# Kernel optimization log

Hardware: AMD Instinct MI355X
Metric: run time of the kernel (lower is better)

Reference implementation:

```python
import jax, jax.numpy as jnp
import numpy as np


def setup_inputs() -> dict:
    key = jax.random.key(0)
    k1, k2, k3, k4, k5 = jax.random.split(key, 5)
    B, N, M, D = 4096, 2048, 2048, 9
    return {
        "x": jax.random.normal(k1, (B, N), dtype=jnp.float32),
        "eternal_weights": jax.random.normal(k2, (D, N, M), dtype=jnp.float32),
        "eternal_biases": jax.random.normal(k3, (M,), dtype=jnp.float32),
        "classical_weights": jax.random.normal(k4, (N, M), dtype=jnp.float32),
        "classical_biases": jax.random.normal(k5, (M,), dtype=jnp.float32),
    }


def _eternal_probs(eternal_weights, n, m):
    # The gate matrix is cos*I - sin*P + sin*P^T with P the circular shift,
    # so (gate @ s)[i] = cos*s[i] - sin*s[(i+1)%n] + sin*s[(i-1)%n].
    # Vectorize over all m output units at once: state is [m, n].
    state0 = jnp.full((m, n), 1.0 / np.sqrt(n), dtype=eternal_weights.dtype)
    angles = eternal_weights[:, :m, :3]  # [D, m, 3] -- weights[depth, j, 0/1/2]

    def gate(state, angle):  # angle: [m]
        c = jnp.cos(angle)[:, None]
        s = jnp.sin(angle)[:, None]
        return c * state - s * jnp.roll(state, -1, axis=1) + s * jnp.roll(state, 1, axis=1)

    def step(state, ang):  # ang: [m, 3] -- consciousness, intelligence, wisdom
        state = gate(state, ang[:, 0])
        state = gate(state, ang[:, 1])
        state = gate(state, ang[:, 2])
        return state, None

    state, _ = jax.lax.scan(step, state0, angles)
    return jnp.abs(state[:, 0]) ** 2  # [m]


def reference(x, eternal_weights, eternal_biases, classical_weights, classical_biases):
    # eternal_biases exists as a parameter in the original module but is unused in forward.
    n = x.shape[1]
    m = classical_weights.shape[1]
    classical = x @ classical_weights + classical_biases  # [B, m]
    probs = _eternal_probs(eternal_weights, n, m)  # [m], identical for every batch row
    return jnp.tanh(classical + probs[None, :])
```

## Files before the change

kernel.cpp:

```cpp
#include <hip/hip_runtime.h>
#include <hip/hip_fp8.h>
#include <stdint.h>

static constexpr int MM = 4096;
static constexpr int KK = 2048;
static constexpr int NN = 2048;

typedef float floatx16 __attribute__((ext_vector_type(16)));
typedef _Float16 f16x8 __attribute__((ext_vector_type(8)));
typedef unsigned short u16x8 __attribute__((ext_vector_type(8)));
typedef int intx4 __attribute__((ext_vector_type(4)));
typedef int intx8 __attribute__((ext_vector_type(8)));

__device__ __forceinline__ unsigned char f32_to_e4m3(float x) {
  __hip_fp8_e4m3 q(x);
  return (unsigned char)q.__x;
}
__device__ __forceinline__ float fast_tanh(float x) {
  float e = __expf(2.0f * x);
  return 1.0f - 2.0f / (e + 1.0f);
}
__device__ __forceinline__ unsigned short f32_to_f16_bits(float x) {
  union { _Float16 h; unsigned short u; } c; c.h = (_Float16)x;
  return c.u;
}
__device__ __forceinline__ float f16_bits_to_f32(unsigned short u) {
  union { _Float16 h; unsigned short u; } c; c.u = u;
  return (float)c.h;
}


__global__ __launch_bounds__(256) void prepass_kernel(
    const float* __restrict__ x, const float* __restrict__ E,
    const float* __restrict__ W, const float* __restrict__ cb,
    unsigned short* __restrict__ ahi, unsigned char* __restrict__ al8,
    unsigned short* __restrict__ bhi, unsigned char* __restrict__ bl8,
    float* __restrict__ bias2) {
  __shared__ float tile[64][65];
  const int blk = blockIdx.x;
  const int tid = threadIdx.x;

  if (blk < 2048) {
    int idx = blk * 256 + tid;
    int row = idx >> 7;
    int u = idx & 127;
    int g = u >> 2;
    int q = u & 3;
    const float4* s = (const float4*)(x + (size_t)row * KK + u * 16);
    float v[16];
#pragma unroll
    for (int p = 0; p < 4; p++) {
      float4 t = s[p];
      v[p * 4 + 0] = t.x; v[p * 4 + 1] = t.y; v[p * 4 + 2] = t.z; v[p * 4 + 3] = t.w;
    }
    unsigned short h[16];
    union { unsigned char b[16]; unsigned long long d[2]; } loq;
#pragma unroll
    for (int e = 0; e < 16; e++) {
      h[e] = f32_to_f16_bits(v[e]);
      float lo = v[e] - f16_bits_to_f32(h[e]);
      loq.b[e] = f32_to_e4m3(lo * 2048.0f);
    }
    size_t rb = (size_t)row * KK;
#pragma unroll
    for (int cc = 0; cc < 2; cc++) {
      int c8 = q * 2 + cc;
      int phys8 = (c8 + row + (row >> 3)) & 7;
      u16x8 o;
#pragma unroll
      for (int e = 0; e < 8; e++) o[e] = h[cc * 8 + e];
      *(u16x8*)(ahi + rb + g * 64 + phys8 * 8) = o;
    }
    {
      int sw = (row & 3) + ((row >> 2) & 3);
      int cA = (q >> 1) * 2;
      char* lb = (char*)al8 + rb + g * 64;
      *(unsigned long long*)(lb + (((cA + 0) + sw) & 3) * 16 + (q & 1) * 8) = loq.d[0];
      *(unsigned long long*)(lb + (((cA + 1) + sw) & 3) * 16 + (q & 1) * 8) = loq.d[1];
    }
  } else if (blk < 3072) {
    const int wb = blk - 2048;
    const int n0 = (wb & 31) * 64;
    const int k0 = (wb >> 5) * 64;
#pragma unroll
    for (int i = 0; i < 4; i++) {
      int t = tid + i * 256;
      int kr = t >> 4;
      int nc = (t & 15) * 4;
      const float4 vv = *(const float4*)(W + (size_t)(k0 + kr) * NN + n0 + nc);
      tile[nc + 0][kr] = vv.x;
      tile[nc + 1][kr] = vv.y;
      tile[nc + 2][kr] = vv.z;
      tile[nc + 3][kr] = vv.w;
    }
    __syncthreads();
    const int nl = tid >> 2;
    const int q = tid & 3;
    const int n = n0 + nl;
    float v[16];
    unsigned short h[16];
    union { unsigned char b[16]; unsigned long long d[2]; } loq;
#pragma unroll
    for (int e = 0; e < 16; e++) {
      v[e] = tile[nl][q * 16 + e];
      h[e] = f32_to_f16_bits(v[e]);
      float lo = v[e] - f16_bits_to_f32(h[e]);
      loq.b[e] = f32_to_e4m3(lo * 2048.0f);
    }
    size_t rb = (size_t)n * KK + k0;
#pragma unroll
    for (int cc = 0; cc < 2; cc++) {
      int c8 = q * 2 + cc;
      int phys8 = (c8 + n + (n >> 3)) & 7;
      u16x8 o;
#pragma unroll
      for (int e = 0; e < 8; e++) o[e] = h[cc * 8 + e];
      *(u16x8*)(bhi + rb + phys8 * 8) = o;
    }
    {
      int sw = (n & 3) + ((n >> 2) & 3);
      int cA = (q >> 1) * 2;
      char* lb = (char*)bl8 + rb;
      *(unsigned long long*)(lb + (((cA + 0) + sw) & 3) * 16 + (q & 1) * 8) = loq.d[0];
      *(unsigned long long*)(lb + (((cA + 1) + sw) & 3) * 16 + (q & 1) * 8) = loq.d[1];
    }
  } else {
    int i = (blk - 3072) * 256 + tid;
    if (i < NN) {
      float p = 1.0f / 2048.0f;
#pragma unroll
      for (int d = 0; d < 9; d++) {
        const float4 a = *(const float4*)(E + (size_t)d * (2048 * 2048) + (size_t)i * 2048);
        float c0 = cosf(a.x), c1 = cosf(a.y), c2 = cosf(a.z);
        p *= (c0 * c0) * (c1 * c1) * (c2 * c2);
      }
      bias2[i] = cb[i] + p;
    }
  }
}

#define GLL(dst, src)                                                        \
  __builtin_amdgcn_global_load_lds(                                          \
      (const __attribute__((address_space(1))) void*)(src),                  \
      (__attribute__((address_space(3))) void*)(dst), 16, 0, 0)

#define BODY(CUR, NXT, KLO, KNX)                                               \
  {                                                                            \
    __builtin_amdgcn_s_barrier();                                              \
    __builtin_amdgcn_sched_barrier(0);                                         \
    _Pragma("unroll") for (int p = 0; p < 2; p++) {                            \
      GLL(&sAl[p * 4096 + lds8], Al8 + a8b + (size_t)(KLO) + (size_t)(64 * p) * KK); \
      GLL(&sBl[p * 4096 + lds8], Bl8 + b8b + (size_t)(KLO) + (size_t)(64 * p) * KK); \
    }                                                                          \
    _Pragma("unroll") for (int p = 0; p < 4; p++) {                            \
      GLL(&sAh[NXT][p * 2048 + lds16], Ahi + a16 + (size_t)(KNX) + (size_t)(32 * p) * KK); \
      GLL(&sBh[NXT][p * 2048 + lds16], Bhi + b16 + (size_t)(KNX) + (size_t)(32 * p) * KK); \
    }                                                                          \
    asm volatile("s_waitcnt vmcnt(12)" ::: "memory");                          \
    __builtin_amdgcn_sched_barrier(0);                                         \
    __builtin_amdgcn_s_barrier();                                              \
    __builtin_amdgcn_sched_barrier(0);                                         \
    intx8 fa8[2], fb8[2];                                                      \
    __builtin_amdgcn_s_setprio(1);                                             \
    _Pragma("unroll") for (int s = 0; s < 4; s++) {                            \
      f16x8 fa[2], fb[2];                                                      \
      _Pragma("unroll") for (int t = 0; t < 2; t++) {                          \
        fa[t] = *(const f16x8*)(sAhB + (CUR) * 16384 + aho[s][t]);             \
        fb[t] = *(const f16x8*)(sBhB + (CUR) * 16384 + bho[s][t]);             \
      }                                                                        \
      _Pragma("unroll") for (int i = 0; i < 2; i++)                            \
        _Pragma("unroll") for (int j = 0; j < 2; j++)                          \
          acc[i][j] = __builtin_amdgcn_mfma_f32_32x32x16_f16(fa[i], fb[j], acc[i][j], 0, 0, 0); \
      _Pragma("unroll") for (int t = 0; t < 2; t++) {                          \
        const uint4 ua = *(const uint4*)&fa[t];                                \
        fa8[t][2 * s]     = (int)__builtin_amdgcn_perm(ua.y, ua.x, 0x07050301u); \
        fa8[t][2 * s + 1] = (int)__builtin_amdgcn_perm(ua.w, ua.z, 0x07050301u); \
        const uint4 ub = *(const uint4*)&fb[t];                                \
        fb8[t][2 * s]     = (int)__builtin_amdgcn_perm(ub.y, ub.x, 0x07050301u); \
        fb8[t][2 * s + 1] = (int)__builtin_amdgcn_perm(ub.w, ub.z, 0x07050301u); \
      }                                                                        \
    }                                                                          \
    __builtin_amdgcn_s_setprio(0);                                             \
    asm volatile("s_waitcnt vmcnt(8)" ::: "memory");                           \
    __builtin_amdgcn_sched_barrier(0);                                         \
    __builtin_amdgcn_s_barrier();                                              \
    __builtin_amdgcn_sched_barrier(0);                                         \
    intx8 fal[2], fbl[2];                                                      \
    _Pragma("unroll") for (int t = 0; t < 2; t++) {                            \
      ((intx4*)&fal[t])[0] = *(const intx4*)(sAlB + alo[t][0]);                \
      ((intx4*)&fal[t])[1] = *(const intx4*)(sAlB + alo[t][1]);                \
      ((intx4*)&fbl[t])[0] = *(const intx4*)(sBlB + blo[t][0]);                \
      ((intx4*)&fbl[t])[1] = *(const intx4*)(sBlB + blo[t][1]);                \
    }                                                                          \
    __builtin_amdgcn_s_setprio(1);                                             \
    _Pragma("unroll") for (int i = 0; i < 2; i++)                              \
      _Pragma("unroll") for (int j = 0; j < 2; j++)                            \
        acc[i][j] = __builtin_amdgcn_mfma_scale_f32_32x32x64_f8f6f4(           \
            fal[i], fb8[j], acc[i][j], 0, 1, 0, 0x74747474, 0, 0x7f7f7f7f);    \
    _Pragma("unroll") for (int i = 0; i < 2; i++)                              \
      _Pragma("unroll") for (int j = 0; j < 2; j++)                            \
        acc[i][j] = __builtin_amdgcn_mfma_scale_f32_32x32x64_f8f6f4(           \
            fa8[i], fbl[j], acc[i][j], 1, 0, 0, 0x7f7f7f7f, 0, 0x74747474);    \
    __builtin_amdgcn_s_setprio(0);                                             \
  }

__global__ __launch_bounds__(256, 2) void gemm_tanh_kernel(
    const unsigned short* __restrict__ Ahi, const unsigned char* __restrict__ Al8,
    const unsigned short* __restrict__ Bhi, const unsigned char* __restrict__ Bl8,
    const float* __restrict__ bias2, float* __restrict__ out) {
  __shared__ __align__(16) unsigned short sAh[2][8192];
  __shared__ __align__(16) unsigned short sBh[2][8192];
  __shared__ __align__(16) unsigned char sAl[8192];
  __shared__ __align__(16) unsigned char sBl[8192];

  const int tid = threadIdx.x;
  const int lane = tid & 63;
  const int wave = tid >> 6;
  const int wm = (wave >> 1) * 64;
  const int wn = (wave & 1) * 64;

  const int id = blockIdx.x;
  const int cid = id >> 4, lid = id & 15;
  const int bm = ((cid >> 2) * 4 + (lid >> 2)) * 128;
  const int bn = ((cid & 3) * 4 + (lid & 3)) * 128;

  const size_t a16 = (size_t)(bm + (tid >> 3)) * KK + (tid & 7) * 8;
  const size_t b16 = (size_t)(bn + (tid >> 3)) * KK + (tid & 7) * 8;
  const size_t a8b = (size_t)(bm + (tid >> 2)) * KK + (tid & 3) * 16;
  const size_t b8b = (size_t)(bn + (tid >> 2)) * KK + (tid & 3) * 16;
  const int lds16 = tid * 8;
  const int lds8 = tid * 16;

  const int r31 = lane & 31;
  const int half = lane >> 5;

  const char* sAhB = (const char*)(&sAh[0][0]);
  const char* sBhB = (const char*)(&sBh[0][0]);
  const char* sAlB = (const char*)(&sAl[0]);
  const char* sBlB = (const char*)(&sBl[0]);
  int aho[4][2], bho[4][2];
#pragma unroll
  for (int s = 0; s < 4; s++)
#pragma unroll
    for (int t = 0; t < 2; t++) {
      const int rowA = wm + t * 32 + r31;
      aho[s][t] = rowA * 128 + ((2 * s + half + rowA + (rowA >> 3)) & 7) * 16;
      const int rowB = wn + t * 32 + r31;
      bho[s][t] = rowB * 128 + ((2 * s + half + rowB + (rowB >> 3)) & 7) * 16;
    }
  int alo[2][2], blo[2][2];
#pragma unroll
  for (int t = 0; t < 2; t++) {
    const int rowA = wm + t * 32 + r31;
    const int swA = (rowA & 3) + ((rowA >> 2) & 3);
    alo[t][0] = rowA * 64 + ((half + swA) & 3) * 16;
    alo[t][1] = rowA * 64 + ((2 + half + swA) & 3) * 16;
    const int rowB = wn + t * 32 + r31;
    const int swB = (rowB & 3) + ((rowB >> 2) & 3);
    blo[t][0] = rowB * 64 + ((half + swB) & 3) * 16;
    blo[t][1] = rowB * 64 + ((2 + half + swB) & 3) * 16;
  }

  floatx16 acc[2][2];
#pragma unroll
  for (int i = 0; i < 2; i++)
#pragma unroll
    for (int j = 0; j < 2; j++)
#pragma unroll
      for (int r = 0; r < 16; r++) acc[i][j][r] = 0.f;

#pragma unroll
  for (int p = 0; p < 4; p++) {
    GLL(&sAh[0][p * 2048 + lds16], Ahi + a16 + (size_t)(32 * p) * KK);
    GLL(&sBh[0][p * 2048 + lds16], Bhi + b16 + (size_t)(32 * p) * KK);
  }

  for (int kt = 0; kt < 32; kt += 2) {
    const int k0 = kt * 64;
    BODY(0, 1, k0, k0 + 64)
    BODY(1, 0, k0 + 64, (kt < 30) ? (k0 + 128) : 0)
  }
  asm volatile("s_waitcnt vmcnt(0)" ::: "memory");

#pragma unroll
  for (int j = 0; j < 2; j++) {
    int col = bn + wn + j * 32 + r31;
    float b2 = bias2[col];
#pragma unroll
    for (int i = 0; i < 2; i++) {
      int row0 = bm + wm + i * 32 + 4 * half;
#pragma unroll
      for (int r = 0; r < 16; r++) {
        int row = row0 + (r & 3) + 8 * (r >> 2);
        float val = acc[i][j][r] + b2;
        __builtin_nontemporal_store(fast_tanh(val), &out[(size_t)row * NN + col]);
      }
    }
  }
}

__global__ __launch_bounds__(256) void fallback_gemm(
    const float* __restrict__ x, const float* __restrict__ E,
    const float* __restrict__ W, const float* __restrict__ cb,
    float* __restrict__ out) {
  __shared__ float sA[16][16];
  __shared__ float sB[16][17];
  __shared__ float sbias[16];
  const int tx = threadIdx.x, ty = threadIdx.y;
  const int row = blockIdx.y * 16 + ty;
  const int col = blockIdx.x * 16 + tx;
  if (ty == 0) {
    float p = 1.0f / 2048.0f;
    for (int d = 0; d < 9; d++) {
      const float* a = E + (size_t)d * (2048 * 2048) + (size_t)col * 2048;
      for (int t = 0; t < 3; t++) { float c = cosf(a[t]); p *= c * c; }
    }
    sbias[tx] = p + cb[col];
  }
  float acc = 0.f;
  for (int k0 = 0; k0 < KK; k0 += 16) {
    __syncthreads();
    sA[ty][tx] = x[(size_t)row * KK + k0 + tx];
    sB[ty][tx] = W[(size_t)(k0 + ty) * NN + col];
    __syncthreads();
#pragma unroll
    for (int kk = 0; kk < 16; kk++) acc += sA[ty][kk] * sB[kk][tx];
  }
  out[(size_t)row * NN + col] = tanhf(acc + sbias[tx]);
}

extern "C" void kernel_launch(void* const* d_in, const int* in_sizes, int n_in,
                              void* d_out, int out_size, void* d_ws, size_t ws_size,
                              hipStream_t stream) {
  const float* x  = (const float*)d_in[0];
  const float* E  = (const float*)d_in[1];
  const float* W  = (const float*)d_in[3];
  const float* cb = (const float*)d_in[4];
  float* out = (float*)d_out;

  const size_t MB = 1024 * 1024;
  const size_t need = 36 * MB + NN * sizeof(float);
  if (ws_size < need) {
    fallback_gemm<<<dim3(NN / 16, MM / 16), dim3(16, 16), 0, stream>>>(x, E, W, cb, out);
    return;
  }

  char* ws = (char*)d_ws;
  unsigned short* Ahi = (unsigned short*)(ws);
  unsigned short* Bhi = (unsigned short*)(ws + 16 * MB);
  unsigned char* Al8  = (unsigned char*)(ws + 24 * MB);
  unsigned char* Bl8  = (unsigned char*)(ws + 32 * MB);
  float* bias2 = (float*)(ws + 36 * MB);

  prepass_kernel<<<dim3(3080), dim3(256), 0, stream>>>(
      x, E, W, cb, Ahi, Al8, Bhi, Bl8, bias2);
  gemm_tanh_kernel<<<dim3(512), dim3(256), 0, stream>>>(
      Ahi, Al8, Bhi, Bl8, bias2, out);
}
```

Before: 295.0 us.

## Use 128x256 tiles with 8 waves and load fp8 residuals straight from global

The GEMM block tile grows from 128x128 with 4 waves to 128x256 with 8 waves, so each A tile is reused across more columns. The fp8 low-part fragments are now loaded from global memory straight into registers instead of being staged through LDS, which removes the LDS buffers for them and one barrier per iteration. The grid shrinks to 256 blocks and the swizzled block ordering is dropped. In exchange, the direct global loads have uncoalesced per-row access, and the smaller grid may leave compute units underused.

```diff
diff --git a/kernel.cpp b/kernel.cpp
--- a/kernel.cpp
+++ b/kernel.cpp
@@ -146,19 +146,25 @@
 
 #define BODY(CUR, NXT, KLO, KNX)                                               \
   {                                                                            \
-    __builtin_amdgcn_s_barrier();                                              \
+    __builtin_amdgcn_s_barrier();    \
     __builtin_amdgcn_sched_barrier(0);                                         \
-    _Pragma("unroll") for (int p = 0; p < 2; p++) {                            \
-      GLL(&sAl[p * 4096 + lds8], Al8 + a8b + (size_t)(KLO) + (size_t)(64 * p) * KK); \
-      GLL(&sBl[p * 4096 + lds8], Bl8 + b8b + (size_t)(KLO) + (size_t)(64 * p) * KK); \
-    }                                                                          \
-    _Pragma("unroll") for (int p = 0; p < 4; p++) {                            \
-      GLL(&sAh[NXT][p * 2048 + lds16], Ahi + a16 + (size_t)(KNX) + (size_t)(32 * p) * KK); \
-      GLL(&sBh[NXT][p * 2048 + lds16], Bhi + b16 + (size_t)(KNX) + (size_t)(32 * p) * KK); \
-    }                                                                          \
-    asm volatile("s_waitcnt vmcnt(12)" ::: "memory");                          \
+       \
+       \
+    intx4 la[2][2], lb[2][2];                                                  \
+    _Pragma("unroll") for (int t = 0; t < 2; t++)                              \
+      _Pragma("unroll") for (int c = 0; c < 2; c++) {                          \
+        la[t][c] = *(const intx4*)(aloP[t][c] + (KLO));                        \
+        lb[t][c] = *(const intx4*)(bloP[t][c] + (KLO));                        \
+      }                                                                        \
     __builtin_amdgcn_sched_barrier(0);                                         \
-    __builtin_amdgcn_s_barrier();                                              \
+                                    \
+    _Pragma("unroll") for (int p = 0; p < 2; p++)                              \
+      GLL(&sAh[NXT][p * 4096 + lds16], Ahi + a16 + (size_t)(KNX) + (size_t)(64 * p) * KK); \
+    _Pragma("unroll") for (int p = 0; p < 4; p++)                              \
+      GLL(&sBh[NXT][p * 4096 + lds16], Bhi + b16 + (size_t)(KNX) + (size_t)(64 * p) * KK); \
+    asm volatile("s_waitcnt vmcnt(14)" ::: "memory");        \
+    __builtin_amdgcn_sched_barrier(0);                                         \
+    __builtin_amdgcn_s_barrier();           \
     __builtin_amdgcn_sched_barrier(0);                                         \
     intx8 fa8[2], fb8[2];                                                      \
     __builtin_amdgcn_s_setprio(1);                                             \
@@ -166,7 +172,7 @@
       f16x8 fa[2], fb[2];                                                      \
       _Pragma("unroll") for (int t = 0; t < 2; t++) {                          \
         fa[t] = *(const f16x8*)(sAhB + (CUR) * 16384 + aho[s][t]);             \
-        fb[t] = *(const f16x8*)(sBhB + (CUR) * 16384 + bho[s][t]);             \
+        fb[t] = *(const f16x8*)(sBhB + (CUR) * 32768 + bho[s][t]);             \
       }                                                                        \
       _Pragma("unroll") for (int i = 0; i < 2; i++)                            \
         _Pragma("unroll") for (int j = 0; j < 2; j++)                          \
@@ -180,19 +186,13 @@
         fb8[t][2 * s + 1] = (int)__builtin_amdgcn_perm(ub.w, ub.z, 0x07050301u); \
       }                                                                        \
     }                                                                          \
-    __builtin_amdgcn_s_setprio(0);                                             \
-    asm volatile("s_waitcnt vmcnt(8)" ::: "memory");                           \
-    __builtin_amdgcn_sched_barrier(0);                                         \
-    __builtin_amdgcn_s_barrier();                                              \
-    __builtin_amdgcn_sched_barrier(0);                                         \
     intx8 fal[2], fbl[2];                                                      \
     _Pragma("unroll") for (int t = 0; t < 2; t++) {                            \
-      ((intx4*)&fal[t])[0] = *(const intx4*)(sAlB + alo[t][0]);                \
-      ((intx4*)&fal[t])[1] = *(const intx4*)(sAlB + alo[t][1]);                \
-      ((intx4*)&fbl[t])[0] = *(const intx4*)(sBlB + blo[t][0]);                \
-      ((intx4*)&fbl[t])[1] = *(const intx4*)(sBlB + blo[t][1]);                \
+      ((intx4*)&fal[t])[0] = la[t][0];                                         \
+      ((intx4*)&fal[t])[1] = la[t][1];                                         \
+      ((intx4*)&fbl[t])[0] = lb[t][0];                                         \
+      ((intx4*)&fbl[t])[1] = lb[t][1];                                         \
     }                                                                          \
-    __builtin_amdgcn_s_setprio(1);                                             \
     _Pragma("unroll") for (int i = 0; i < 2; i++)                              \
       _Pragma("unroll") for (int j = 0; j < 2; j++)                            \
         acc[i][j] = __builtin_amdgcn_mfma_scale_f32_32x32x64_f8f6f4(           \
@@ -204,40 +204,32 @@
     __builtin_amdgcn_s_setprio(0);                                             \
   }
 
-__global__ __launch_bounds__(256, 2) void gemm_tanh_kernel(
+__global__ __launch_bounds__(512, 2) void gemm_tanh_kernel(
     const unsigned short* __restrict__ Ahi, const unsigned char* __restrict__ Al8,
     const unsigned short* __restrict__ Bhi, const unsigned char* __restrict__ Bl8,
     const float* __restrict__ bias2, float* __restrict__ out) {
   __shared__ __align__(16) unsigned short sAh[2][8192];
-  __shared__ __align__(16) unsigned short sBh[2][8192];
-  __shared__ __align__(16) unsigned char sAl[8192];
-  __shared__ __align__(16) unsigned char sBl[8192];
+  __shared__ __align__(16) unsigned short sBh[2][16384];
 
   const int tid = threadIdx.x;
   const int lane = tid & 63;
   const int wave = tid >> 6;
-  const int wm = (wave >> 1) * 64;
-  const int wn = (wave & 1) * 64;
+  const int wm = (wave >> 2) * 64;
+  const int wn = (wave & 3) * 64;
 
   const int id = blockIdx.x;
-  const int cid = id >> 4, lid = id & 15;
-  const int bm = ((cid >> 2) * 4 + (lid >> 2)) * 128;
-  const int bn = ((cid & 3) * 4 + (lid & 3)) * 128;
+  const int bm = (id >> 3) * 128;
+  const int bn = (id & 7) * 256;
 
   const size_t a16 = (size_t)(bm + (tid >> 3)) * KK + (tid & 7) * 8;
   const size_t b16 = (size_t)(bn + (tid >> 3)) * KK + (tid & 7) * 8;
-  const size_t a8b = (size_t)(bm + (tid >> 2)) * KK + (tid & 3) * 16;
-  const size_t b8b = (size_t)(bn + (tid >> 2)) * KK + (tid & 3) * 16;
   const int lds16 = tid * 8;
-  const int lds8 = tid * 16;
 
   const int r31 = lane & 31;
   const int half = lane >> 5;
 
   const char* sAhB = (const char*)(&sAh[0][0]);
   const char* sBhB = (const char*)(&sBh[0][0]);
-  const char* sAlB = (const char*)(&sAl[0]);
-  const char* sBlB = (const char*)(&sBl[0]);
   int aho[4][2], bho[4][2];
 #pragma unroll
   for (int s = 0; s < 4; s++)
@@ -248,17 +240,18 @@
       const int rowB = wn + t * 32 + r31;
       bho[s][t] = rowB * 128 + ((2 * s + half + rowB + (rowB >> 3)) & 7) * 16;
     }
-  int alo[2][2], blo[2][2];
+  const char* aloP[2][2];
+  const char* bloP[2][2];
 #pragma unroll
   for (int t = 0; t < 2; t++) {
     const int rowA = wm + t * 32 + r31;
     const int swA = (rowA & 3) + ((rowA >> 2) & 3);
-    alo[t][0] = rowA * 64 + ((half + swA) & 3) * 16;
-    alo[t][1] = rowA * 64 + ((2 + half + swA) & 3) * 16;
+    aloP[t][0] = (const char*)Al8 + (size_t)(bm + rowA) * KK + ((half + swA) & 3) * 16;
+    aloP[t][1] = (const char*)Al8 + (size_t)(bm + rowA) * KK + ((2 + half + swA) & 3) * 16;
     const int rowB = wn + t * 32 + r31;
     const int swB = (rowB & 3) + ((rowB >> 2) & 3);
-    blo[t][0] = rowB * 64 + ((half + swB) & 3) * 16;
-    blo[t][1] = rowB * 64 + ((2 + half + swB) & 3) * 16;
+    bloP[t][0] = (const char*)Bl8 + (size_t)(bn + rowB) * KK + ((half + swB) & 3) * 16;
+    bloP[t][1] = (const char*)Bl8 + (size_t)(bn + rowB) * KK + ((2 + half + swB) & 3) * 16;
   }
 
   floatx16 acc[2][2];
@@ -270,10 +263,11 @@
       for (int r = 0; r < 16; r++) acc[i][j][r] = 0.f;
 
 #pragma unroll
-  for (int p = 0; p < 4; p++) {
-    GLL(&sAh[0][p * 2048 + lds16], Ahi + a16 + (size_t)(32 * p) * KK);
-    GLL(&sBh[0][p * 2048 + lds16], Bhi + b16 + (size_t)(32 * p) * KK);
-  }
+  for (int p = 0; p < 2; p++)
+    GLL(&sAh[0][p * 4096 + lds16], Ahi + a16 + (size_t)(64 * p) * KK);
+#pragma unroll
+  for (int p = 0; p < 4; p++)
+    GLL(&sBh[0][p * 4096 + lds16], Bhi + b16 + (size_t)(64 * p) * KK);
 
   for (int kt = 0; kt < 32; kt += 2) {
     const int k0 = kt * 64;
@@ -354,6 +348,6 @@
 
   prepass_kernel<<<dim3(3080), dim3(256), 0, stream>>>(
       x, E, W, cb, Ahi, Al8, Bhi, Bl8, bias2);
-  gemm_tanh_kernel<<<dim3(512), dim3(256), 0, stream>>>(
+  gemm_tanh_kernel<<<dim3(256), dim3(512), 0, stream>>>(
       Ahi, Al8, Bhi, Bl8, bias2, out);
 }
```

Result: slower. 312.6 us (+6.0%).
